# Kernel tuning notes

Hardware: AMD Instinct MI355X
Metric: run time of the kernel (lower is better)

Reference implementation:

```python
import jax, jax.numpy as jnp
import numpy as np

N, E, H, D_IN, D_OUT, DEPTH, G = 100000, 1600000, 128, 128, 10, 3, 256


def setup_inputs() -> dict:
    key = jax.random.key(0)
    ks = jax.random.split(key, 16)
    s = lambda k, shape: jax.random.normal(k, shape, dtype=jnp.float32) * 0.05
    inp = {
        "x": jax.random.normal(ks[0], (N, D_IN), dtype=jnp.float32),
        "edge_index": jax.random.randint(ks[1], (2, E), 0, N, dtype=jnp.int32),
        "control_edge_index": jax.random.randint(ks[2], (2, 1024), 0, N, dtype=jnp.int32),
        "batch": jnp.sort(jax.random.randint(ks[3], (N,), 0, G, dtype=jnp.int32)),
        # encoder MLP: input_dim -> hidden -> hidden
        "enc_w1": s(ks[4], (D_IN, H)), "enc_b1": jnp.zeros((H,), jnp.float32),
        "enc_w2": s(ks[5], (H, H)),    "enc_b2": jnp.zeros((H,), jnp.float32),
        # conv_depth GCN layers, hidden -> hidden
        "conv_w": s(ks[6], (DEPTH, H, H)), "conv_b": jnp.zeros((DEPTH, H), jnp.float32),
        # decoder MLP: hidden -> hidden -> output_dim
        "dec_w1": s(ks[7], (H, H)),     "dec_b1": jnp.zeros((H,), jnp.float32),
        "dec_w2": s(ks[8], (H, D_OUT)), "dec_b2": jnp.zeros((D_OUT,), jnp.float32),
    }
    return inp


def _gcn_forward(x, enc_w1, enc_b1, enc_w2, enc_b2, conv_w, conv_b,
                 dec_w1, dec_b1, dec_w2, dec_b2, edge_index, batch):
    # encoder MLP (Linear-ReLU-Dropout(eval)-Linear)
    h = jax.nn.relu(x @ enc_w1 + enc_b1) @ enc_w2 + enc_b2

    # GCN normalization with self-loops: D^{-1/2} (A + I) D^{-1/2}
    loops = jnp.arange(N, dtype=edge_index.dtype)
    src = jnp.concatenate([edge_index[0], loops])  # [E + N]
    dst = jnp.concatenate([edge_index[1], loops])
    deg = jax.ops.segment_sum(jnp.ones_like(src, dtype=h.dtype), dst, num_segments=N)
    inv_sqrt = jax.lax.rsqrt(deg)  # deg >= 1 thanks to self-loops
    coef = (inv_sqrt[src] * inv_sqrt[dst])[:, None]  # [E+N, 1]

    for l in range(DEPTH):
        hw = h @ conv_w[l] + conv_b[l]                      # [N, H]
        h = jax.ops.segment_sum(hw[src] * coef, dst, num_segments=N)
        if l < DEPTH - 1:  # linear=False -> nonlinearity between convs
            h = jax.nn.relu(h)

    # global_add_pool over graph ids
    pooled = jax.ops.segment_sum(h, batch, num_segments=G)   # [G, H]

    # decoder MLP
    return jax.nn.relu(pooled @ dec_w1 + dec_b1) @ dec_w2 + dec_b2  # [G, D_OUT]


def reference(x, edge_index, control_edge_index, batch, enc_w1, enc_b1, enc_w2,
              enc_b2, conv_w, conv_b, dec_w1, dec_b1, dec_w2, dec_b2):
    # control_edge_index corresponds to the (disabled) control mechanism; unused
    return _gcn_forward(x, enc_w1, enc_b1, enc_w2, enc_b2, conv_w, conv_b,
                        dec_w1, dec_b1, dec_w2, dec_b2, edge_index, batch)
```

## Files before the change

kernel.cpp:

```cpp
#include <hip/hip_runtime.h>
#include <hip/hip_bf16.h>
#include <cstdint>
#include <cstddef>

#define NN 100000
#define NE 1600000
#define HH 128
#define NG 256

#define NB 196
#define BSH 9
#define BMSK 511
#define CHUNK 16384
#define NBLK 98

typedef __bf16 bf16x8 __attribute__((ext_vector_type(8)));
typedef float floatx4 __attribute__((ext_vector_type(4)));

__device__ __forceinline__ uint32_t f2b(float f) {
  union { float f; uint32_t u; } v; v.f = f;
  uint32_t u = v.u;
  return (u + 0x7FFFu + ((u >> 16) & 1u)) >> 16;
}
__device__ __forceinline__ float b2f(uint32_t h) {
  union { uint32_t u; float f; } v; v.u = h << 16;
  return v.f;
}
__device__ __forceinline__ float blo(uint32_t u) {
  union { uint32_t u; float f; } v; v.u = u << 16;
  return v.f;
}
__device__ __forceinline__ float bhi(uint32_t u) {
  union { uint32_t u; float f; } v; v.u = u & 0xFFFF0000u;
  return v.f;
}
__device__ __forceinline__ void addrow(float* a, uint4 v) {
  a[0] += blo(v.x); a[1] += bhi(v.x);
  a[2] += blo(v.y); a[3] += bhi(v.y);
  a[4] += blo(v.z); a[5] += bhi(v.z);
  a[6] += blo(v.w); a[7] += bhi(v.w);
}

__device__ __forceinline__ void stage_w(uint16_t (*Wt)[136], const float* __restrict__ W,
                                        int tid) {
  for (int it = 0; it < 16; ++it) {
    int idx = tid + it * 256;
    int n = idx & 127;
    int k0 = (idx >> 7) * 4;
    uint2 wv;
    wv.x = f2b(W[(k0 + 0) * 128 + n]) | (f2b(W[(k0 + 1) * 128 + n]) << 16);
    wv.y = f2b(W[(k0 + 2) * 128 + n]) | (f2b(W[(k0 + 3) * 128 + n]) << 16);
    *(uint2*)&Wt[n][k0] = wv;
  }
}


__global__ __launch_bounds__(256) void k_cntA(const int* __restrict__ src,
                                              int* __restrict__ blkcnt) {
  __shared__ int h[NB];
  int t = threadIdx.x;
  if (t < NB) h[t] = 0;
  __syncthreads();
  int base = blockIdx.x * CHUNK, end = min(base + CHUNK, NE);
  for (int i = base + t; i < end; i += 256) atomicAdd(&h[src[i] >> BSH], 1);
  __syncthreads();
  if (t < NB) blkcnt[blockIdx.x * NB + t] = h[t];
}

__global__ __launch_bounds__(256) void k_cntB(const uint2* __restrict__ pairs,
                                              int* __restrict__ blkcnt) {
  __shared__ int h[NB];
  int t = threadIdx.x;
  if (t < NB) h[t] = 0;
  __syncthreads();
  int base = blockIdx.x * CHUNK, end = min(base + CHUNK, NE);
  for (int i = base + t; i < end; i += 256) atomicAdd(&h[pairs[i].y >> BSH], 1);
  __syncthreads();
  if (t < NB) blkcnt[blockIdx.x * NB + t] = h[t];
}

__global__ void k_scan(const int* __restrict__ blkcnt, int* __restrict__ poff,
                       int* __restrict__ gbase, int* __restrict__ off, int set_off) {
  __shared__ int s[256];
  int t = threadIdx.x;
  int tot = 0;
  if (t < NB) {
    for (int r = 0; r < NBLK; ++r) {
      poff[r * NB + t] = tot;
      tot += blkcnt[r * NB + t];
    }
  }
  s[t] = (t < NB) ? tot : 0;
  __syncthreads();
  for (int d = 1; d < 256; d <<= 1) {
    int v = (t >= d) ? s[t - d] : 0;
    __syncthreads();
    s[t] += v;
    __syncthreads();
  }
  if (t < NB) gbase[t] = s[t] - tot;
  if (t == 0) { gbase[NB] = NE; if (set_off) off[NN] = NE; }
}

__global__ __launch_bounds__(256) void k_placeA(const int* __restrict__ src,
                                                const int* __restrict__ dst,
                                                const int* __restrict__ poff,
                                                const int* __restrict__ gbase,
                                                uint2* __restrict__ pairs) {
  __shared__ int cur[NB];
  int t = threadIdx.x;
  if (t < NB) cur[t] = poff[blockIdx.x * NB + t] + gbase[t];
  __syncthreads();
  int base = blockIdx.x * CHUNK, end = min(base + CHUNK, NE);
  for (int i = base + t; i < end; i += 256) {
    int s = src[i], d = dst[i];
    int p = atomicAdd(&cur[s >> BSH], 1);
    pairs[p] = make_uint2((unsigned)s, (unsigned)d);
  }
}

__global__ __launch_bounds__(256) void k_placeB(const uint2* __restrict__ pairs,
                                                const int* __restrict__ poff,
                                                const int* __restrict__ gbase,
                                                uint32_t* __restrict__ outb) {
  __shared__ int cur[NB];
  int t = threadIdx.x;
  if (t < NB) cur[t] = poff[blockIdx.x * NB + t] + gbase[t];
  __syncthreads();
  int base = blockIdx.x * CHUNK, end = min(base + CHUNK, NE);
  for (int i = base + t; i < end; i += 256) {
    uint2 v = pairs[i];
    int p = atomicAdd(&cur[v.y >> BSH], 1);
    outb[p] = v.x | ((v.y & (unsigned)BMSK) << 17);
  }
}

__global__ __launch_bounds__(256) void k_bucket_sort(
    const uint32_t* __restrict__ pairbuf, const int* __restrict__ gbase,
    const int* __restrict__ batch,
    int* __restrict__ off, float* __restrict__ inv, int* __restrict__ csrs,
    int* __restrict__ dhist2, int* __restrict__ gstart)
{
  __shared__ int cnt[512];
  __shared__ int loff[512];
  __shared__ int psum[256];
  int b = blockIdx.x;
  int tid = threadIdx.x;
  cnt[tid] = 0; cnt[tid + 256] = 0;
  __syncthreads();
  int s0 = gbase[b], s1 = gbase[b + 1];
  for (int i = s0 + tid; i < s1; i += 256)
    atomicAdd(&cnt[pairbuf[i] >> 17], 1);
  __syncthreads();
  int a0 = cnt[2 * tid], a1 = cnt[2 * tid + 1];
  int s = a0 + a1;
  psum[tid] = s;
  __syncthreads();
  for (int d = 1; d < 256; d <<= 1) {
    int v = (tid >= d) ? psum[tid - d] : 0;
    __syncthreads();
    psum[tid] += v;
    __syncthreads();
  }
  int excl = psum[tid] - s;
  loff[2 * tid] = excl;
  loff[2 * tid + 1] = excl + a0;
  __syncthreads();
  int* h64 = psum;
  if (tid < 64) h64[tid] = 0;
  __syncthreads();
#pragma unroll
  for (int k = 0; k < 2; ++k) {
    int i = tid + k * 256;
    int node = b * 512 + i;
    if (node < NN) {
      off[node] = s0 + loff[i];
      inv[node] = rsqrtf((float)cnt[i] + 1.0f);
      int d = cnt[i]; if (d > 63) d = 63;
      atomicAdd(&h64[d], 1);
    }
  }
  {
    int n0 = b * 512, n1 = min(n0 + 512, NN);
    for (int i = n0 + tid; i < n1; i += 256) {
      int bb = batch[i];
      if (i == 0) { for (int g = 0; g <= bb; ++g) gstart[g] = 0; }
      else { int aa = batch[i - 1]; for (int g = aa + 1; g <= bb; ++g) gstart[g] = i; }
      if (i == NN - 1) { for (int g = bb + 1; g <= NG; ++g) gstart[g] = NN; }
    }
  }
  __syncthreads();
  if (tid < 64) dhist2[b * 64 + tid] = h64[tid];
  cnt[tid] = loff[tid]; cnt[tid + 256] = loff[tid + 256];
  __syncthreads();
  for (int i = s0 + tid; i < s1; i += 256) {
    uint32_t v = pairbuf[i];
    int p = atomicAdd(&cnt[v >> 17], 1);
    csrs[s0 + p] = (int)(v & 0x1FFFFu);
  }
}

__global__ void k_dscan(const int* __restrict__ dhist2, int* __restrict__ dcur) {
  int t = threadIdx.x;
  int sum = 0;
  for (int r = 0; r < NB; ++r) sum += dhist2[r * 64 + (63 - t)];
  int v = sum;
  for (int d = 1; d < 64; d <<= 1) { int u = __shfl_up(v, d); if (t >= d) v += u; }
  dcur[63 - t] = v - sum;
}

__global__ __launch_bounds__(256) void k_dplace(const int* __restrict__ off,
                                                int* __restrict__ dcur,
                                                int* __restrict__ order) {
  __shared__ int h[64], base[64];
  int t = threadIdx.x;
  if (t < 64) h[t] = 0;
  __syncthreads();
  int i = blockIdx.x * 256 + t;
  int d = 0, ld = 0;
  if (i < NN) { d = off[i + 1] - off[i]; if (d > 63) d = 63; ld = atomicAdd(&h[d], 1); }
  __syncthreads();
  if (t < 64) base[t] = h[t] ? atomicAdd(&dcur[t], h[t]) : 0;
  __syncthreads();
  if (i < NN) order[base[d] + ld] = i;
}

__global__ __launch_bounds__(256) void k_gemm(
    const uint16_t* __restrict__ A16, const float* __restrict__ A32,
    const float* __restrict__ W, const float* __restrict__ bias,
    const float* __restrict__ scale,
    uint16_t* __restrict__ Out, int M, int do_relu)
{
  __shared__ uint16_t Wt[128][136];
  const int tid = threadIdx.x;
  stage_w(Wt, W, tid);
  __syncthreads();

  const int lane = tid & 63;
  const int wave = tid >> 6;
  const int lrow = lane & 15;
  const int quad = lane >> 4;
  const int lk = quad * 8;
  const int row0 = blockIdx.x * 128 + wave * 32;

  floatx4 acc[2][8];
#pragma unroll
  for (int t = 0; t < 2; ++t)
#pragma unroll
    for (int n = 0; n < 8; ++n)
      acc[t][n] = (floatx4){0.f, 0.f, 0.f, 0.f};

#pragma unroll
  for (int ks = 0; ks < 4; ++ks) {
    bf16x8 a[2];
#pragma unroll
    for (int t = 0; t < 2; ++t) {
      int r = row0 + t * 16 + lrow;
      uint4 tmp = {0u, 0u, 0u, 0u};
      if (r < M) {
        if (A32) {
          float4 f0 = *(const float4*)(A32 + (size_t)r * HH + ks * 32 + lk);
          float4 f1 = *(const float4*)(A32 + (size_t)r * HH + ks * 32 + lk + 4);
          tmp.x = f2b(f0.x) | (f2b(f0.y) << 16);
          tmp.y = f2b(f0.z) | (f2b(f0.w) << 16);
          tmp.z = f2b(f1.x) | (f2b(f1.y) << 16);
          tmp.w = f2b(f1.z) | (f2b(f1.w) << 16);
        } else {
          tmp = *(const uint4*)(A16 + (size_t)r * HH + ks * 32 + lk);
        }
      }
      a[t] = __builtin_bit_cast(bf16x8, tmp);
    }
#pragma unroll
    for (int n = 0; n < 8; ++n) {
      bf16x8 b = __builtin_bit_cast(bf16x8, *(const uint4*)&Wt[n * 16 + lrow][ks * 32 + lk]);
      acc[0][n] = __builtin_amdgcn_mfma_f32_16x16x32_bf16(b, a[0], acc[0][n], 0, 0, 0);
      acc[1][n] = __builtin_amdgcn_mfma_f32_16x16x32_bf16(b, a[1], acc[1][n], 0, 0, 0);
    }
  }

  float4 b4[8];
#pragma unroll
  for (int n = 0; n < 8; ++n) b4[n] = *(const float4*)(bias + n * 16 + quad * 4);

#pragma unroll
  for (int t = 0; t < 2; ++t) {
    int row = row0 + t * 16 + lrow;
    if (row < M) {
      float sc = scale ? scale[row] : 1.0f;
      uint16_t* orow = Out + (size_t)row * HH;
#pragma unroll
      for (int n = 0; n < 8; ++n) {
        float v0 = acc[t][n][0] + b4[n].x;
        float v1 = acc[t][n][1] + b4[n].y;
        float v2 = acc[t][n][2] + b4[n].z;
        float v3 = acc[t][n][3] + b4[n].w;
        if (do_relu) {
          v0 = fmaxf(v0, 0.f); v1 = fmaxf(v1, 0.f);
          v2 = fmaxf(v2, 0.f); v3 = fmaxf(v3, 0.f);
        }
        v0 *= sc; v1 *= sc; v2 *= sc; v3 *= sc;
        uint2 o;
        o.x = f2b(v0) | (f2b(v1) << 16);
        o.y = f2b(v2) | (f2b(v3) << 16);
        *(uint2*)(orow + n * 16 + quad * 4) = o;
      }
    }
  }
}

__global__ __launch_bounds__(256) void k_gemm_dual(
    const uint16_t* __restrict__ A16,
    const float* __restrict__ Wa, const float* __restrict__ ba,
    const float* __restrict__ Wb, const float* __restrict__ bb,
    const float* __restrict__ scale,
    uint16_t* __restrict__ Out, int M)
{
  __shared__ uint16_t Wt[128][136];
  __shared__ uint16_t tile[128][136];
  const int tid = threadIdx.x;
  stage_w(Wt, Wa, tid);
  __syncthreads();

  const int lane = tid & 63;
  const int wave = tid >> 6;
  const int lrow = lane & 15;
  const int quad = lane >> 4;
  const int lk = quad * 8;
  const int row0 = blockIdx.x * 128 + wave * 32;
  const int trow0 = wave * 32;

  floatx4 acc[2][8];
#pragma unroll
  for (int t = 0; t < 2; ++t)
#pragma unroll
    for (int n = 0; n < 8; ++n)
      acc[t][n] = (floatx4){0.f, 0.f, 0.f, 0.f};

#pragma unroll
  for (int ks = 0; ks < 4; ++ks) {
    bf16x8 a[2];
#pragma unroll
    for (int t = 0; t < 2; ++t) {
      int r = row0 + t * 16 + lrow;
      uint4 tmp = {0u, 0u, 0u, 0u};
      if (r < M) tmp = *(const uint4*)(A16 + (size_t)r * HH + ks * 32 + lk);
      a[t] = __builtin_bit_cast(bf16x8, tmp);
    }
#pragma unroll
    for (int n = 0; n < 8; ++n) {
      bf16x8 b = __builtin_bit_cast(bf16x8, *(const uint4*)&Wt[n * 16 + lrow][ks * 32 + lk]);
      acc[0][n] = __builtin_amdgcn_mfma_f32_16x16x32_bf16(b, a[0], acc[0][n], 0, 0, 0);
      acc[1][n] = __builtin_amdgcn_mfma_f32_16x16x32_bf16(b, a[1], acc[1][n], 0, 0, 0);
    }
  }

  {
    float4 b4[8];
#pragma unroll
    for (int n = 0; n < 8; ++n) b4[n] = *(const float4*)(ba + n * 16 + quad * 4);
#pragma unroll
    for (int t = 0; t < 2; ++t) {
      int trow = trow0 + t * 16 + lrow;
#pragma unroll
      for (int n = 0; n < 8; ++n) {
        uint2 o;
        o.x = f2b(acc[t][n][0] + b4[n].x) | (f2b(acc[t][n][1] + b4[n].y) << 16);
        o.y = f2b(acc[t][n][2] + b4[n].z) | (f2b(acc[t][n][3] + b4[n].w) << 16);
        *(uint2*)&tile[trow][n * 16 + quad * 4] = o;
      }
    }
  }
  __syncthreads();
  stage_w(Wt, Wb, tid);
#pragma unroll
  for (int t = 0; t < 2; ++t)
#pragma unroll
    for (int n = 0; n < 8; ++n)
      acc[t][n] = (floatx4){0.f, 0.f, 0.f, 0.f};
  __syncthreads();

#pragma unroll
  for (int ks = 0; ks < 4; ++ks) {
    bf16x8 a[2];
#pragma unroll
    for (int t = 0; t < 2; ++t)
      a[t] = __builtin_bit_cast(bf16x8,
               *(const uint4*)&tile[trow0 + t * 16 + lrow][ks * 32 + lk]);
#pragma unroll
    for (int n = 0; n < 8; ++n) {
      bf16x8 b = __builtin_bit_cast(bf16x8, *(const uint4*)&Wt[n * 16 + lrow][ks * 32 + lk]);
      acc[0][n] = __builtin_amdgcn_mfma_f32_16x16x32_bf16(b, a[0], acc[0][n], 0, 0, 0);
      acc[1][n] = __builtin_amdgcn_mfma_f32_16x16x32_bf16(b, a[1], acc[1][n], 0, 0, 0);
    }
  }

  {
    float4 b4[8];
#pragma unroll
    for (int n = 0; n < 8; ++n) b4[n] = *(const float4*)(bb + n * 16 + quad * 4);
#pragma unroll
    for (int t = 0; t < 2; ++t) {
      int row = row0 + t * 16 + lrow;
      if (row < M) {
        float sc = scale ? scale[row] : 1.0f;
        uint16_t* orow = Out + (size_t)row * HH;
#pragma unroll
        for (int n = 0; n < 8; ++n) {
          float v0 = (acc[t][n][0] + b4[n].x) * sc;
          float v1 = (acc[t][n][1] + b4[n].y) * sc;
          float v2 = (acc[t][n][2] + b4[n].z) * sc;
          float v3 = (acc[t][n][3] + b4[n].w) * sc;
          uint2 o;
          o.x = f2b(v0) | (f2b(v1) << 16);
          o.y = f2b(v2) | (f2b(v3) << 16);
          *(uint2*)(orow + n * 16 + quad * 4) = o;
        }
      }
    }
  }
}

__global__ __launch_bounds__(256) void k_agg(
    const uint16_t* __restrict__ hw2, const int* __restrict__ off,
    const int* __restrict__ csrs, const float* __restrict__ inv,
    const int* __restrict__ order,
    uint16_t* __restrict__ hout, int do_relu)
{
  int slot = blockIdx.x * 16 + (threadIdx.x >> 4);
  if (slot >= NN) return;
  int node = order[slot];
  int c = (threadIdx.x & 15) * 8;
  const uint16_t* rowp = hw2 + c;

  uint4 sv = *(const uint4*)(rowp + (size_t)node * HH);
  float a[8] = {0.f, 0.f, 0.f, 0.f, 0.f, 0.f, 0.f, 0.f};
  addrow(a, sv);

  int e0 = off[node], e1 = off[node + 1];
  int e = e0;
  if (e + 4 <= e1) {
    int i0 = csrs[e + 0], i1 = csrs[e + 1], i2 = csrs[e + 2], i3 = csrs[e + 3];
    uint4 v0 = *(const uint4*)(rowp + (size_t)i0 * HH);
    uint4 v1 = *(const uint4*)(rowp + (size_t)i1 * HH);
    uint4 v2 = *(const uint4*)(rowp + (size_t)i2 * HH);
    uint4 v3 = *(const uint4*)(rowp + (size_t)i3 * HH);
    for (e += 4; e + 4 <= e1; e += 4) {
      int j0 = csrs[e + 0], j1 = csrs[e + 1], j2 = csrs[e + 2], j3 = csrs[e + 3];
      uint4 w0 = *(const uint4*)(rowp + (size_t)j0 * HH);
      uint4 w1 = *(const uint4*)(rowp + (size_t)j1 * HH);
      uint4 w2 = *(const uint4*)(rowp + (size_t)j2 * HH);
      uint4 w3 = *(const uint4*)(rowp + (size_t)j3 * HH);
      addrow(a, v0); addrow(a, v1); addrow(a, v2); addrow(a, v3);
      v0 = w0; v1 = w1; v2 = w2; v3 = w3;
    }
    addrow(a, v0); addrow(a, v1); addrow(a, v2); addrow(a, v3);
  }
  for (; e < e1; ++e) {
    int s = csrs[e];
    uint4 v = *(const uint4*)(rowp + (size_t)s * HH);
    addrow(a, v);
  }
  float invd = inv[node];
#pragma unroll
  for (int j = 0; j < 8; ++j) {
    a[j] *= invd;
    if (do_relu) a[j] = fmaxf(a[j], 0.f);
  }
  uint4 o;
  o.x = f2b(a[0]) | (f2b(a[1]) << 16);
  o.y = f2b(a[2]) | (f2b(a[3]) << 16);
  o.z = f2b(a[4]) | (f2b(a[5]) << 16);
  o.w = f2b(a[6]) | (f2b(a[7]) << 16);
  *(uint4*)(hout + (size_t)node * HH + c) = o;
}

__global__ __launch_bounds__(256) void k_pooldec(
    const uint16_t* __restrict__ h, const int* __restrict__ gstart,
    const float* __restrict__ w1, const float* __restrict__ b1,
    const float* __restrict__ w2, const float* __restrict__ b2,
    float* __restrict__ out)
{
  __shared__ float red[16][132];
  __shared__ float p[128], tmpv[128];
  int g = blockIdx.x;
  int tid = threadIdx.x;
  int slot = tid >> 4;
  int c = (tid & 15) * 8;

  int r0 = gstart[g], r1 = gstart[g + 1];
  float a[8] = {0.f, 0.f, 0.f, 0.f, 0.f, 0.f, 0.f, 0.f};
  for (int r = r0 + slot; r < r1; r += 16) {
    uint4 v = *(const uint4*)(h + (size_t)r * HH + c);
    addrow(a, v);
  }
  *(float4*)&red[slot][c]     = make_float4(a[0], a[1], a[2], a[3]);
  *(float4*)&red[slot][c + 4] = make_float4(a[4], a[5], a[6], a[7]);
  __syncthreads();
  if (tid < 128) {
    float s = 0.f;
#pragma unroll
    for (int k = 0; k < 16; ++k) s += red[k][tid];
    p[tid] = s;
  }
  __syncthreads();
  if (tid < 128) {
    float acc1 = b1[tid];
    for (int k = 0; k < 128; ++k) acc1 += p[k] * w1[k * 128 + tid];
    tmpv[tid] = fmaxf(acc1, 0.f);
  }
  __syncthreads();
  if (tid < 10) {
    float o = b2[tid];
    for (int k = 0; k < 128; ++k) o += tmpv[k] * w2[k * 10 + tid];
    out[g * 10 + tid] = o;
  }
}

extern "C" void kernel_launch(void* const* d_in, const int* in_sizes, int n_in,
                              void* d_out, int out_size, void* d_ws, size_t ws_size,
                              hipStream_t stream) {
  const float* x       = (const float*)d_in[0];
  const int*   eidx    = (const int*)d_in[1];
  const int*   src     = eidx;
  const int*   dst     = eidx + NE;
  const int*   batch   = (const int*)d_in[3];
  const float* enc_w1  = (const float*)d_in[4];
  const float* enc_b1  = (const float*)d_in[5];
  const float* enc_w2  = (const float*)d_in[6];
  const float* enc_b2  = (const float*)d_in[7];
  const float* conv_w  = (const float*)d_in[8];
  const float* conv_b  = (const float*)d_in[9];
  const float* dec_w1  = (const float*)d_in[10];
  const float* dec_b1  = (const float*)d_in[11];
  const float* dec_w2  = (const float*)d_in[12];
  const float* dec_b2  = (const float*)d_in[13];
  float* out = (float*)d_out;

  char* ws = (char*)d_ws;
  size_t o = 0;
  auto alloc = [&](size_t bytes) -> char* {
    char* p = ws + o;
    o += (bytes + 255) & ~(size_t)255;
    return p;
  };
  int*      off     = (int*)alloc((size_t)(NN + 1) * 4);
  int*      csrs    = (int*)alloc((size_t)NE * 4);
  float*    inv     = (float*)alloc((size_t)NN * 4);
  int*      blkcntA = (int*)alloc((size_t)NBLK * NB * 4);
  int*      poffA   = (int*)alloc((size_t)NBLK * NB * 4);
  int*      blkcntB = (int*)alloc((size_t)NBLK * NB * 4);
  int*      poffB   = (int*)alloc((size_t)NBLK * NB * 4);
  int*      gbaseA  = (int*)alloc((size_t)(NB + 1) * 4);
  int*      gbaseB  = (int*)alloc((size_t)(NB + 1) * 4);
  int*      dhist2  = (int*)alloc((size_t)NB * 64 * 4);
  int*      dcur    = (int*)alloc(64 * 4);
  int*      order   = (int*)alloc((size_t)NN * 4);
  int*      gstart  = (int*)alloc((size_t)(NG + 1) * 4);
  uint16_t* buf0    = (uint16_t*)alloc((size_t)NN * HH * 2);
  uint16_t* buf1    = (uint16_t*)alloc((size_t)NN * HH * 2);
  uint2*    pairsA  = (uint2*)buf1;
  uint32_t* pairB   = (uint32_t*)((char*)buf1 + (size_t)NE * 8);

  k_cntA<<<dim3(NBLK), dim3(256), 0, stream>>>(src, blkcntA);
  k_scan<<<dim3(1), dim3(256), 0, stream>>>(blkcntA, poffA, gbaseA, off, 0);
  k_placeA<<<dim3(NBLK), dim3(256), 0, stream>>>(src, dst, poffA, gbaseA, pairsA);
  k_cntB<<<dim3(NBLK), dim3(256), 0, stream>>>(pairsA, blkcntB);
  k_scan<<<dim3(1), dim3(256), 0, stream>>>(blkcntB, poffB, gbaseB, off, 1);
  k_placeB<<<dim3(NBLK), dim3(256), 0, stream>>>(pairsA, poffB, gbaseB, pairB);
  k_bucket_sort<<<dim3(NB), dim3(256), 0, stream>>>(pairB, gbaseB, batch, off, inv, csrs,
                                                    dhist2, gstart);

  const int NBK = (NN + 255) / 256;
  k_dscan<<<dim3(1), dim3(64), 0, stream>>>(dhist2, dcur);
  k_dplace<<<dim3(NBK), dim3(256), 0, stream>>>(off, dcur, order);

  const int GB = (NN + 127) / 128;
  k_gemm<<<dim3(GB), dim3(256), 0, stream>>>(nullptr, x, enc_w1, enc_b1, nullptr, buf1, NN, 1);
  k_gemm_dual<<<dim3(GB), dim3(256), 0, stream>>>(buf1, enc_w2, enc_b2,
                                                  conv_w + 0 * 16384, conv_b + 0,
                                                  inv, buf0, NN);

  const int AB = (NN + 15) / 16;
  k_agg <<<dim3(AB), dim3(256), 0, stream>>>(buf0, off, csrs, inv, order, buf1, 1);
  k_gemm<<<dim3(GB), dim3(256), 0, stream>>>(buf1, nullptr, conv_w + 1 * 16384, conv_b + 128, inv, buf0, NN, 0);
  k_agg <<<dim3(AB), dim3(256), 0, stream>>>(buf0, off, csrs, inv, order, buf1, 1);
  k_gemm<<<dim3(GB), dim3(256), 0, stream>>>(buf1, nullptr, conv_w + 2 * 16384, conv_b + 256, inv, buf0, NN, 0);
  k_agg <<<dim3(AB), dim3(256), 0, stream>>>(buf0, off, csrs, inv, order, buf1, 0);

  k_pooldec<<<dim3(NG), dim3(256), 0, stream>>>(buf1, gstart, dec_w1, dec_b1, dec_w2, dec_b2, out);
}
```

Baseline: 519.4 us.

## Fuse GCN aggregation with following layer GEMM in one kernel

Adds a kernel that gathers neighbour rows for 32 nodes per block, stages the ReLU'd aggregated rows in shared memory, and immediately multiplies them by the next conv weight with MFMA, writing the scaled result. This replaces the two agg+gemm pairs for layers 1 and 2, removing a round trip of the N×H intermediate through global memory and two launches. It also simplifies the gather loop by dropping the software-pipelined prefetch. Each block re-stages and converts the full weight matrix, which adds per-block overhead, and the launch assumes N is divisible by 32.

```diff
diff --git a/kernel.cpp b/kernel.cpp
--- a/kernel.cpp
+++ b/kernel.cpp
@@ -21,10 +21,6 @@
   union { float f; uint32_t u; } v; v.f = f;
   uint32_t u = v.u;
   return (u + 0x7FFFu + ((u >> 16) & 1u)) >> 16;
-}
-__device__ __forceinline__ float b2f(uint32_t h) {
-  union { uint32_t u; float f; } v; v.u = h << 16;
-  return v.f;
 }
 __device__ __forceinline__ float blo(uint32_t u) {
   union { uint32_t u; float f; } v; v.u = u << 16;
@@ -439,21 +435,12 @@
 
   int e0 = off[node], e1 = off[node + 1];
   int e = e0;
-  if (e + 4 <= e1) {
-    int i0 = csrs[e + 0], i1 = csrs[e + 1], i2 = csrs[e + 2], i3 = csrs[e + 3];
-    uint4 v0 = *(const uint4*)(rowp + (size_t)i0 * HH);
-    uint4 v1 = *(const uint4*)(rowp + (size_t)i1 * HH);
-    uint4 v2 = *(const uint4*)(rowp + (size_t)i2 * HH);
-    uint4 v3 = *(const uint4*)(rowp + (size_t)i3 * HH);
-    for (e += 4; e + 4 <= e1; e += 4) {
-      int j0 = csrs[e + 0], j1 = csrs[e + 1], j2 = csrs[e + 2], j3 = csrs[e + 3];
-      uint4 w0 = *(const uint4*)(rowp + (size_t)j0 * HH);
-      uint4 w1 = *(const uint4*)(rowp + (size_t)j1 * HH);
-      uint4 w2 = *(const uint4*)(rowp + (size_t)j2 * HH);
-      uint4 w3 = *(const uint4*)(rowp + (size_t)j3 * HH);
-      addrow(a, v0); addrow(a, v1); addrow(a, v2); addrow(a, v3);
-      v0 = w0; v1 = w1; v2 = w2; v3 = w3;
-    }
+  for (; e + 4 <= e1; e += 4) {
+    int s0 = csrs[e + 0], s1 = csrs[e + 1], s2 = csrs[e + 2], s3 = csrs[e + 3];
+    uint4 v0 = *(const uint4*)(rowp + (size_t)s0 * HH);
+    uint4 v1 = *(const uint4*)(rowp + (size_t)s1 * HH);
+    uint4 v2 = *(const uint4*)(rowp + (size_t)s2 * HH);
+    uint4 v3 = *(const uint4*)(rowp + (size_t)s3 * HH);
     addrow(a, v0); addrow(a, v1); addrow(a, v2); addrow(a, v3);
   }
   for (; e < e1; ++e) {
@@ -473,6 +460,100 @@
   o.z = f2b(a[4]) | (f2b(a[5]) << 16);
   o.w = f2b(a[6]) | (f2b(a[7]) << 16);
   *(uint4*)(hout + (size_t)node * HH + c) = o;
+}
+
+__global__ __launch_bounds__(512) void k_aggemm(
+    const uint16_t* __restrict__ hw2, const int* __restrict__ off,
+    const int* __restrict__ csrs, const float* __restrict__ inv,
+    const int* __restrict__ order,
+    const float* __restrict__ W, const float* __restrict__ bias,
+    uint16_t* __restrict__ Out)
+{
+  __shared__ uint16_t Wt[128][136];
+  __shared__ uint16_t S[32][136];
+  __shared__ int nid[32];
+  const int tid = threadIdx.x;
+
+  for (int it = 0; it < 8; ++it) {
+    int idx = tid + it * 512;
+    int n = idx & 127;
+    int k0 = (idx >> 7) * 4;
+    uint2 wv;
+    wv.x = f2b(W[(k0 + 0) * 128 + n]) | (f2b(W[(k0 + 1) * 128 + n]) << 16);
+    wv.y = f2b(W[(k0 + 2) * 128 + n]) | (f2b(W[(k0 + 3) * 128 + n]) << 16);
+    *(uint2*)&Wt[n][k0] = wv;
+  }
+
+  const int group = tid >> 4;
+  const int node = order[blockIdx.x * 32 + group];
+  const int c = (tid & 15) * 8;
+  if ((tid & 15) == 0) nid[group] = node;
+  const uint16_t* rowp = hw2 + c;
+
+  uint4 sv = *(const uint4*)(rowp + (size_t)node * HH);
+  float a[8] = {0.f, 0.f, 0.f, 0.f, 0.f, 0.f, 0.f, 0.f};
+  addrow(a, sv);
+
+  int e0 = off[node], e1 = off[node + 1];
+  int e = e0;
+  for (; e + 4 <= e1; e += 4) {
+    int s0 = csrs[e + 0], s1 = csrs[e + 1], s2 = csrs[e + 2], s3 = csrs[e + 3];
+    uint4 v0 = *(const uint4*)(rowp + (size_t)s0 * HH);
+    uint4 v1 = *(const uint4*)(rowp + (size_t)s1 * HH);
+    uint4 v2 = *(const uint4*)(rowp + (size_t)s2 * HH);
+    uint4 v3 = *(const uint4*)(rowp + (size_t)s3 * HH);
+    addrow(a, v0); addrow(a, v1); addrow(a, v2); addrow(a, v3);
+  }
+  for (; e < e1; ++e) {
+    int s = csrs[e];
+    uint4 v = *(const uint4*)(rowp + (size_t)s * HH);
+    addrow(a, v);
+  }
+  float invd = inv[node];
+#pragma unroll
+  for (int j = 0; j < 8; ++j) a[j] = fmaxf(a[j] * invd, 0.f);
+  {
+    uint4 o;
+    o.x = f2b(a[0]) | (f2b(a[1]) << 16);
+    o.y = f2b(a[2]) | (f2b(a[3]) << 16);
+    o.z = f2b(a[4]) | (f2b(a[5]) << 16);
+    o.w = f2b(a[6]) | (f2b(a[7]) << 16);
+    *(uint4*)&S[group][c] = o;
+  }
+  __syncthreads();
+
+  const int lane = tid & 63;
+  const int wave = tid >> 6;
+  const int lrow = lane & 15;
+  const int quad = lane >> 4;
+  const int lk = quad * 8;
+
+  floatx4 acc0 = (floatx4){0.f, 0.f, 0.f, 0.f};
+  floatx4 acc1 = (floatx4){0.f, 0.f, 0.f, 0.f};
+#pragma unroll
+  for (int ks = 0; ks < 4; ++ks) {
+    bf16x8 a0 = __builtin_bit_cast(bf16x8, *(const uint4*)&S[lrow][ks * 32 + lk]);
+    bf16x8 a1 = __builtin_bit_cast(bf16x8, *(const uint4*)&S[16 + lrow][ks * 32 + lk]);
+    bf16x8 b  = __builtin_bit_cast(bf16x8, *(const uint4*)&Wt[wave * 16 + lrow][ks * 32 + lk]);
+    acc0 = __builtin_amdgcn_mfma_f32_16x16x32_bf16(b, a0, acc0, 0, 0, 0);
+    acc1 = __builtin_amdgcn_mfma_f32_16x16x32_bf16(b, a1, acc1, 0, 0, 0);
+  }
+
+  float4 b4 = *(const float4*)(bias + wave * 16 + quad * 4);
+#pragma unroll
+  for (int t = 0; t < 2; ++t) {
+    floatx4 ac = t ? acc1 : acc0;
+    int row = nid[t * 16 + lrow];
+    float sc = inv[row];
+    float v0 = (ac[0] + b4.x) * sc;
+    float v1 = (ac[1] + b4.y) * sc;
+    float v2 = (ac[2] + b4.z) * sc;
+    float v3 = (ac[3] + b4.w) * sc;
+    uint2 o;
+    o.x = f2b(v0) | (f2b(v1) << 16);
+    o.y = f2b(v2) | (f2b(v3) << 16);
+    *(uint2*)(Out + (size_t)row * HH + wave * 16 + quad * 4) = o;
+  }
 }
 
 __global__ __launch_bounds__(256) void k_pooldec(
@@ -581,11 +662,12 @@
                                                   conv_w + 0 * 16384, conv_b + 0,
                                                   inv, buf0, NN);
 
+  const int FB = NN / 32;
   const int AB = (NN + 15) / 16;
-  k_agg <<<dim3(AB), dim3(256), 0, stream>>>(buf0, off, csrs, inv, order, buf1, 1);
-  k_gemm<<<dim3(GB), dim3(256), 0, stream>>>(buf1, nullptr, conv_w + 1 * 16384, conv_b + 128, inv, buf0, NN, 0);
-  k_agg <<<dim3(AB), dim3(256), 0, stream>>>(buf0, off, csrs, inv, order, buf1, 1);
-  k_gemm<<<dim3(GB), dim3(256), 0, stream>>>(buf1, nullptr, conv_w + 2 * 16384, conv_b + 256, inv, buf0, NN, 0);
+  k_aggemm<<<dim3(FB), dim3(512), 0, stream>>>(buf0, off, csrs, inv, order,
+                                               conv_w + 1 * 16384, conv_b + 128, buf1);
+  k_aggemm<<<dim3(FB), dim3(512), 0, stream>>>(buf1, off, csrs, inv, order,
+                                               conv_w + 2 * 16384, conv_b + 256, buf0);
   k_agg <<<dim3(AB), dim3(256), 0, stream>>>(buf0, off, csrs, inv, order, buf1, 0);
 
   k_pooldec<<<dim3(NG), dim3(256), 0, stream>>>(buf1, gstart, dec_w1, dec_b1, dec_w2, dec_b2, out);
```

Result: faster. 497.1 us (-4.3%).
